# Performance work log

Hardware: AMD Instinct MI355X
Metric: run time of the kernel (lower is better)

The kernel has to match this reference:

```python
import jax, jax.numpy as jnp
import numpy as np

B, D, H = 16384, 1024, 4096


def setup_inputs() -> dict:
    key = jax.random.key(0)
    kx, kp, k1, k2 = jax.random.split(key, 4)
    X = jax.random.normal(kx, (B, D), dtype=jnp.float32)
    prot_col_idx = 3
    # protected column must be binary {0,1} so the remap produces no NaNs
    prot = jax.random.randint(kp, (B,), 0, 2).astype(jnp.float32)
    X = X.at[:, prot_col_idx].set(prot)
    W1 = jax.random.normal(k1, (D, H), dtype=jnp.float32) * (1.0 / np.sqrt(D))
    b1 = jnp.zeros((H,), dtype=jnp.float32)
    W2 = jax.random.normal(k2, (H, D), dtype=jnp.float32) * (1.0 / np.sqrt(H))
    b2 = jnp.zeros((D,), dtype=jnp.float32)
    return {"X": X, "W1": W1, "b1": b1, "W2": W2, "b2": b2,
            "prot_col_idx": prot_col_idx}


def reference(X, W1, b1, W2, b2, prot_col_idx):
    def explainer(x):
        h = jnp.tanh(x @ W1 + b1)          # [B, H]
        return h @ W2 + b2                  # [B, D]

    # vectorized remap of the protected column: 0 -> 1, 1 -> 0, else NaN
    col = X[:, prot_col_idx]
    flipped = jnp.where(col == 0, jnp.float32(1.0),
                        jnp.where(col == 1, jnp.float32(0.0), jnp.float32(jnp.nan)))
    X_copy = X.at[:, prot_col_idx].set(flipped.astype(X.dtype))

    shaps = explainer(X)
    shaps_counter = explainer(X_copy)
    mean_euclid_dist = jnp.mean(jnp.abs(shaps - shaps_counter), axis=0)  # [D]
    return mean_euclid_dist.sum()
```

## Files before the change

### kernel.cpp

```cpp
#include <hip/hip_runtime.h>
#include <stdint.h>

#define B_N 16384
#define D_N 1024
#define H_N 4096

typedef int i32x4 __attribute__((ext_vector_type(4)));
typedef int i32x8 __attribute__((ext_vector_type(8)));
typedef float f32x4 __attribute__((ext_vector_type(4)));

__device__ __forceinline__ void gload16(const void* g, void* l) {
  __builtin_amdgcn_global_load_lds((const __attribute__((address_space(1))) void*)g,
                                   (__attribute__((address_space(3))) void*)l,
                                   16, 0, 0);
}

__device__ __forceinline__ unsigned char f2fp8(float v) {
  return (unsigned char)(__builtin_amdgcn_cvt_pk_fp8_f32(v, v, 0, false) & 0xFF);
}

__device__ __forceinline__ int perm_h(int h) {
  return (h & ~63) | ((h & 15) << 2) | ((h >> 4) & 3);
}

__device__ __forceinline__ void transpose_tile(
    const float* __restrict__ in, unsigned char* __restrict__ out,
    int R, int C, float scale, float* __restrict__ w3, int pci,
    int i0, int j0, int tx, int ty, bool permute) {
  __shared__ float tile[32][33];
#pragma unroll
  for (int r = 0; r < 32; r += 8) {
    int i = i0 + ty + r;
    int j = j0 + tx;
    float v = in[(size_t)i * C + j];
    tile[ty + r][tx] = v;
    if (w3 != nullptr && i == pci) w3[j] = v;
  }
  __syncthreads();
#pragma unroll
  for (int r = 0; r < 32; r += 8) {
    int jo = j0 + ty + r;
    int io = i0 + tx;
    int ioo = permute ? perm_h(io) : io;
    out[(size_t)jo * R + ioo] = f2fp8(tile[tx][ty + r] * scale);
  }
}

__global__ __launch_bounds__(256) void prep_kernel(
    const float4* __restrict__ X4, int* __restrict__ Xb,
    float* __restrict__ s,
    const float* __restrict__ W1, unsigned char* __restrict__ W1T, float* __restrict__ w3,
    const float* __restrict__ W2, unsigned char* __restrict__ W2T,
    const int* __restrict__ pci_p, float* __restrict__ out0) {
  int b = blockIdx.x;
  int tid = threadIdx.x;
  int pci = *pci_p;
  if (b == 0 && tid == 0) out0[0] = 0.0f;
  if (b < 8192) {
    int i = (b * 256 + tid) * 2;
#pragma unroll
    for (int u = 0; u < 2; u++) {
      float4 v = X4[i + u];
      int p = __builtin_amdgcn_cvt_pk_fp8_f32(v.x, v.y, 0, false);
      p = __builtin_amdgcn_cvt_pk_fp8_f32(v.z, v.w, p, true);
      Xb[i + u] = p;
      if (((i + u) & (D_N / 4 - 1)) == (pci >> 2)) {
        int row = (i + u) >> 8;
        float c;
        switch (pci & 3) {
          case 0:  c = v.x; break;
          case 1:  c = v.y; break;
          case 2:  c = v.z; break;
          default: c = v.w; break;
        }
        s[row] = 1.0f - 2.0f * c;
      }
    }
  } else if (b < 12288) {
    int id = b - 8192;
    transpose_tile(W1, W1T, D_N, H_N, 16.0f, w3, pci,
                   (id >> 7) * 32, (id & 127) * 32, tid & 31, tid >> 5, false);
  } else {
    int id = b - 12288;
    transpose_tile(W2, W2T, H_N, D_N, 64.0f, nullptr, -1,
                   (id >> 5) * 32, (id & 31) * 32, tid & 31, tid >> 5, true);
  }
}

template <int KTOT>
__device__ __forceinline__ void mx_mainloop(
    const unsigned char* __restrict__ A, const unsigned char* __restrict__ B,
    int m0, int n0, int sa, int sb,
    unsigned char* As, unsigned char* Bs, f32x4 (&acc)[4][4]) {
  const int tid = threadIdx.x;
  const int lane = tid & 63;
  const int wave = tid >> 6;
  const int wm = (wave >> 1) * 64;
  const int wn = (wave & 1) * 64;
  const int lm = lane & 15;
  const int quad = lane >> 4;

  const int srow = tid >> 3;
  const int clog = (tid & 7) ^ (srow & 7);
  const unsigned char* Ag = A + (size_t)(m0 + srow) * KTOT + clog * 16;
  const unsigned char* Bg = B + (size_t)(n0 + srow) * KTOT + clog * 16;
  unsigned char* As_l = As + tid * 16;
  unsigned char* Bs_l = Bs + tid * 16;

  for (int k0 = 0; k0 < KTOT; k0 += 128) {
#pragma unroll
    for (int it = 0; it < 4; it++) {
      gload16(Ag + k0 + (size_t)(32 * it) * KTOT, As_l + it * 4096);
      gload16(Bg + k0 + (size_t)(32 * it) * KTOT, Bs_l + it * 4096);
    }
    __syncthreads();
    i32x8 b[4];
#pragma unroll
    for (int j = 0; j < 4; j++) {
      int r = wn + j * 16 + lm;
      int e = r & 7;
      i32x4 lo = *(const i32x4*)&Bs[r * 128 + ((2 * quad) ^ e) * 16];
      i32x4 hi = *(const i32x4*)&Bs[r * 128 + ((2 * quad + 1) ^ e) * 16];
      b[j] = __builtin_shufflevector(lo, hi, 0, 1, 2, 3, 4, 5, 6, 7);
    }
#pragma unroll
    for (int i = 0; i < 4; i++) {
      int r = wm + i * 16 + lm;
      int e = r & 7;
      i32x4 lo = *(const i32x4*)&As[r * 128 + ((2 * quad) ^ e) * 16];
      i32x4 hi = *(const i32x4*)&As[r * 128 + ((2 * quad + 1) ^ e) * 16];
      i32x8 av = __builtin_shufflevector(lo, hi, 0, 1, 2, 3, 4, 5, 6, 7);
#pragma unroll
      for (int j = 0; j < 4; j++)
        acc[i][j] = __builtin_amdgcn_mfma_scale_f32_16x16x128_f8f6f4(
            av, b[j], acc[i][j], 0, 0, 0, sa, 0, sb);
    }
    __syncthreads();
  }
}

__global__ __launch_bounds__(256, 4) void gemm1_dh(
    const unsigned char* __restrict__ Xb,
    const unsigned char* __restrict__ W1T,
    const float* __restrict__ b1,
    const float* __restrict__ w3,
    const float* __restrict__ s,
    unsigned int* __restrict__ Dh4) {
  __shared__ alignas(16) unsigned char As[128 * 128];
  __shared__ alignas(16) unsigned char Bs[128 * 128];
  int l = blockIdx.y * gridDim.x + blockIdx.x;
  int x = l & 7;
  int k = l >> 3;
  int ni = k & 7;
  int m  = (k >> 3) & 15;
  int nc = k >> 7;
  const int m0 = (x * 16 + m) * 128;
  const int n0 = (nc * 8 + ni) * 128;

  f32x4 acc[4][4] = {};
  mx_mainloop<D_N>(Xb, W1T, m0, n0, 127, 123, As, Bs, acc);

  const int tid = threadIdx.x;
  const int lane = tid & 63;
  const int wave = tid >> 6;
  const int wm = (wave >> 1) * 64;
  const int wn = (wave & 1) * 64;
  const int lm = lane & 15;
  const int quad = lane >> 4;

  float ewp[4], ewm[4], nump[4], numm[4], b1v[4];
#pragma unroll
  for (int j = 0; j < 4; j++) {
    int gh = n0 + wn + j * 16 + lm;
    float w = w3[gh];
    float ep = __expf(2.0f * w);
    float em = __expf(-2.0f * w);
    ewp[j] = ep; ewm[j] = em;
    nump[j] = 128.0f * (1.0f - ep);
    numm[j] = 128.0f * (1.0f - em);
    b1v[j] = b1[gh];
  }
  const size_t coloff = (size_t)((n0 + wn) >> 2) + lm;
#pragma unroll
  for (int i = 0; i < 4; i++) {
#pragma unroll
    for (int r = 0; r < 4; r++) {
      int gb = m0 + wm + i * 16 + quad * 4 + r;
      bool sp = s[gb] > 0.0f;
      float o[4];
#pragma unroll
      for (int j = 0; j < 4; j++) {
        float ews = sp ? ewp[j] : ewm[j];
        float num = sp ? nump[j] : numm[j];
        float z = fminf(acc[i][j][r] + b1v[j], 12.0f);
        float E = __expf(2.0f * z);
        float den = (E * ews + 1.0f) * (E + 1.0f);
        o[j] = (E * num) * __builtin_amdgcn_rcpf(den);
      }
      int p = __builtin_amdgcn_cvt_pk_fp8_f32(o[0], o[1], 0, false);
      p = __builtin_amdgcn_cvt_pk_fp8_f32(o[2], o[3], p, true);
      Dh4[(size_t)gb * (H_N / 4) + coloff] = (unsigned int)p;
    }
  }
}

__global__ __launch_bounds__(256, 4) void gemm2_abs(
    const unsigned char* __restrict__ Dh,
    const unsigned char* __restrict__ W2T,
    float* __restrict__ out) {
  __shared__ alignas(16) unsigned char As[128 * 128];
  __shared__ alignas(16) unsigned char Bs[128 * 128];
  __shared__ float wsum[4];
  int l = blockIdx.y * gridDim.x + blockIdx.x;
  int x = l & 7;
  int k = l >> 3;
  int c = k >> 6;
  int idx = k & 63;
  int m  = idx >> 2;
  int nj = idx & 3;
  const int m0 = (x * 16 + m) * 128;
  const int n0 = (c * 4 + nj) * 128;

  f32x4 acc[4][4] = {};
  mx_mainloop<H_N>(Dh, W2T, m0, n0, 121, 121, As, Bs, acc);

  const int tid = threadIdx.x;
  const int lane = tid & 63;
  const int wave = tid >> 6;

  float t = 0.0f;
#pragma unroll
  for (int i = 0; i < 4; i++)
#pragma unroll
    for (int j = 0; j < 4; j++)
#pragma unroll
      for (int r = 0; r < 4; r++)
        t += fabsf(acc[i][j][r]);

#pragma unroll
  for (int off2 = 32; off2 > 0; off2 >>= 1)
    t += __shfl_down(t, off2, 64);
  if (lane == 0) wsum[wave] = t;
  __syncthreads();
  if (tid == 0)
    atomicAdd(out, (wsum[0] + wsum[1] + wsum[2] + wsum[3]) * (1.0f / (float)B_N));
}

extern "C" void kernel_launch(void* const* d_in, const int* in_sizes, int n_in,
                              void* d_out, int out_size, void* d_ws, size_t ws_size,
                              hipStream_t stream) {
  const float* X  = (const float*)d_in[0];
  const float* W1 = (const float*)d_in[1];
  const float* b1 = (const float*)d_in[2];
  const float* W2 = (const float*)d_in[3];
  const int* pci  = (const int*)d_in[5];

  char* ws = (char*)d_ws;
  size_t off = 0;
  unsigned char* Xb  = (unsigned char*)(ws + off); off += (size_t)B_N * D_N;
  unsigned char* W1T = (unsigned char*)(ws + off); off += (size_t)H_N * D_N;
  unsigned char* W2T = (unsigned char*)(ws + off); off += (size_t)D_N * H_N;
  float* w3  = (float*)(ws + off); off += (size_t)H_N * 4;
  float* s   = (float*)(ws + off); off += (size_t)B_N * 4;
  unsigned char* Dh  = (unsigned char*)(ws + off); off += (size_t)B_N * H_N;
  if (ws_size < off) return;

  prep_kernel<<<16384, 256, 0, stream>>>((const float4*)X, (int*)Xb, s,
                                         W1, W1T, w3, W2, W2T, pci,
                                         (float*)d_out);
  gemm1_dh<<<dim3(32, 128), 256, 0, stream>>>(Xb, W1T, b1, w3, s,
                                              (unsigned int*)Dh);
  gemm2_abs<<<dim3(8, 128), 256, 0, stream>>>(Dh, W2T, (float*)d_out);
}
```

Before: 289.8 us.

## Use 256x256 tiles with 8 waves and double-buffered LDS prefetch in FP8 GEMMs

Both MX-FP8 GEMMs move from 128x128 tiles with 4 waves to 256x256 tiles with 8 waves, each wave computing 128x64. The main loop now double-buffers LDS and splits the next K-slab's global-to-LDS loads into chunks that are interleaved with the MFMA groups. It uses explicit vmcnt waits, barriers and s_setprio around the MFMA bursts. The aim is more operand reuse per byte loaded and hiding global load latency behind matrix math. The cost is 128KB of LDS per block, which allows only one block per CU, plus more barriers per K step; gemm2 launches just 256 blocks.

```diff
diff --git a/kernel.cpp b/kernel.cpp
--- a/kernel.cpp
+++ b/kernel.cpp
@@ -88,83 +88,135 @@
 }
 
 template <int KTOT>
-__device__ __forceinline__ void mx_mainloop(
+__device__ __forceinline__ void mx8_mainloop(
     const unsigned char* __restrict__ A, const unsigned char* __restrict__ B,
     int m0, int n0, int sa, int sb,
-    unsigned char* As, unsigned char* Bs, f32x4 (&acc)[4][4]) {
+    unsigned char* __restrict__ As, unsigned char* __restrict__ Bs,
+    f32x4 (&acc)[8][4]) {
+  static_assert(KTOT % 128 == 0, "KTOT must be a multiple of 128");
   const int tid = threadIdx.x;
   const int lane = tid & 63;
   const int wave = tid >> 6;
-  const int wm = (wave >> 1) * 64;
-  const int wn = (wave & 1) * 64;
+  const int wm = (wave >> 2) * 128;
+  const int wn = (wave & 3) * 64;
   const int lm = lane & 15;
   const int quad = lane >> 4;
 
   const int srow = tid >> 3;
-  const int clog = (tid & 7) ^ (srow & 7);
-  const unsigned char* Ag = A + (size_t)(m0 + srow) * KTOT + clog * 16;
-  const unsigned char* Bg = B + (size_t)(n0 + srow) * KTOT + clog * 16;
-  unsigned char* As_l = As + tid * 16;
-  unsigned char* Bs_l = Bs + tid * 16;
-
-  for (int k0 = 0; k0 < KTOT; k0 += 128) {
-#pragma unroll
-    for (int it = 0; it < 4; it++) {
-      gload16(Ag + k0 + (size_t)(32 * it) * KTOT, As_l + it * 4096);
-      gload16(Bg + k0 + (size_t)(32 * it) * KTOT, Bs_l + it * 4096);
-    }
-    __syncthreads();
-    i32x8 b[4];
-#pragma unroll
-    for (int j = 0; j < 4; j++) {
-      int r = wn + j * 16 + lm;
-      int e = r & 7;
-      i32x4 lo = *(const i32x4*)&Bs[r * 128 + ((2 * quad) ^ e) * 16];
-      i32x4 hi = *(const i32x4*)&Bs[r * 128 + ((2 * quad + 1) ^ e) * 16];
-      b[j] = __builtin_shufflevector(lo, hi, 0, 1, 2, 3, 4, 5, 6, 7);
-    }
-#pragma unroll
-    for (int i = 0; i < 4; i++) {
-      int r = wm + i * 16 + lm;
-      int e = r & 7;
-      i32x4 lo = *(const i32x4*)&As[r * 128 + ((2 * quad) ^ e) * 16];
-      i32x4 hi = *(const i32x4*)&As[r * 128 + ((2 * quad + 1) ^ e) * 16];
-      i32x8 av = __builtin_shufflevector(lo, hi, 0, 1, 2, 3, 4, 5, 6, 7);
-#pragma unroll
-      for (int j = 0; j < 4; j++)
-        acc[i][j] = __builtin_amdgcn_mfma_scale_f32_16x16x128_f8f6f4(
-            av, b[j], acc[i][j], 0, 0, 0, sa, 0, sb);
-    }
-    __syncthreads();
-  }
-}
-
-__global__ __launch_bounds__(256, 4) void gemm1_dh(
+  const int sg = tid & 7;
+  const unsigned char* Ag = A + (size_t)(m0 + srow) * KTOT + ((sg ^ (srow & 7)) * 16);
+  const unsigned char* Bg = B + (size_t)(n0 + srow) * KTOT + ((sg ^ (srow & 7)) * 16);
+  unsigned char* AsW = As + tid * 16;
+  unsigned char* BsW = Bs + tid * 16;
+
+#define STGA(c_, k_, p_) gload16(Ag + (k_) + (c_) * 64 * KTOT, AsW + (p_) * 32768 + (c_) * 8192)
+#define STGB(c_, k_, p_) gload16(Bg + (k_) + (c_) * 64 * KTOT, BsW + (p_) * 32768 + (c_) * 8192)
+#define LDF(d_, base_, r_) { \
+    const int rr_ = (r_); \
+    const int e_ = rr_ & 7; \
+    const unsigned char* pp_ = (base_) + rr_ * 128; \
+    i32x4 lo_ = *(const i32x4*)(pp_ + (((2 * quad) ^ e_) * 16)); \
+    i32x4 hi_ = *(const i32x4*)(pp_ + (((2 * quad + 1) ^ e_) * 16)); \
+    d_ = __builtin_shufflevector(lo_, hi_, 0, 1, 2, 3, 4, 5, 6, 7); }
+#define MF(a_, b_, c_) \
+    __builtin_amdgcn_mfma_scale_f32_16x16x128_f8f6f4((a_), (b_), (c_), 0, 0, 0, sa, 0, sb)
+#define FENCE() asm volatile("" ::: "memory")
+#define BARR() { FENCE(); __builtin_amdgcn_s_barrier(); FENCE(); }
+#define MM8(i0_, i1_, aA_, aB_) { \
+    __builtin_amdgcn_s_setprio(1); \
+    acc[i0_][0] = MF(aA_, b0, acc[i0_][0]); \
+    acc[i0_][1] = MF(aA_, b1, acc[i0_][1]); \
+    acc[i0_][2] = MF(aA_, b2, acc[i0_][2]); \
+    acc[i0_][3] = MF(aA_, b3, acc[i0_][3]); \
+    acc[i1_][0] = MF(aB_, b0, acc[i1_][0]); \
+    acc[i1_][1] = MF(aB_, b1, acc[i1_][1]); \
+    acc[i1_][2] = MF(aB_, b2, acc[i1_][2]); \
+    acc[i1_][3] = MF(aB_, b3, acc[i1_][3]); \
+    __builtin_amdgcn_s_setprio(0); }
+
+  STGB(0, 0, 0); STGB(1, 0, 0); STGB(2, 0, 0); STGB(3, 0, 0);
+  STGA(0, 0, 0); STGA(2, 0, 0);
+  STGA(1, 0, 0); STGA(3, 0, 0);
+  asm volatile("s_waitcnt vmcnt(2)" ::: "memory");
+  BARR();
+
+  const int NT = KTOT / 128;
+#pragma unroll 2
+  for (int t = 0; t < NT; ++t) {
+    const unsigned char* Ar = As + (t & 1) * 32768;
+    const unsigned char* Br = Bs + (t & 1) * 32768;
+    const int pq = (t & 1) ^ 1;
+    const int k1 = (t + 1) * 128;
+    const bool pf = (t + 1 < NT);
+
+    i32x8 b0, b1, b2, b3, av0, av1;
+    LDF(b0, Br, wn + lm);
+    LDF(b1, Br, wn + 16 + lm);
+    LDF(b2, Br, wn + 32 + lm);
+    LDF(b3, Br, wn + 48 + lm);
+    LDF(av0, Ar, wm + lm);
+    LDF(av1, Ar, wm + 16 + lm);
+    if (pf) { STGB(0, k1, pq); STGB(1, k1, pq); }
+    BARR();
+    MM8(0, 1, av0, av1);
+    BARR();
+
+    LDF(av0, Ar, wm + 32 + lm);
+    LDF(av1, Ar, wm + 48 + lm);
+    if (pf) { STGB(2, k1, pq); STGB(3, k1, pq); }
+    BARR();
+    MM8(2, 3, av0, av1);
+    if (pf) { asm volatile("s_waitcnt vmcnt(4)" ::: "memory"); }
+    else    { asm volatile("s_waitcnt vmcnt(0)" ::: "memory"); }
+    BARR();
+
+    LDF(av0, Ar, wm + 64 + lm);
+    LDF(av1, Ar, wm + 80 + lm);
+    if (pf) { STGA(0, k1, pq); STGA(2, k1, pq); }
+    BARR();
+    MM8(4, 5, av0, av1);
+    BARR();
+
+    LDF(av0, Ar, wm + 96 + lm);
+    LDF(av1, Ar, wm + 112 + lm);
+    if (pf) { STGA(1, k1, pq); STGA(3, k1, pq); }
+    BARR();
+    MM8(6, 7, av0, av1);
+    if (pf) { asm volatile("s_waitcnt vmcnt(2)" ::: "memory"); }
+    BARR();
+  }
+#undef STGA
+#undef STGB
+#undef LDF
+#undef MF
+#undef FENCE
+#undef BARR
+#undef MM8
+}
+
+__global__ __launch_bounds__(512, 2) void gemm1_dh(
     const unsigned char* __restrict__ Xb,
     const unsigned char* __restrict__ W1T,
     const float* __restrict__ b1,
     const float* __restrict__ w3,
     const float* __restrict__ s,
     unsigned int* __restrict__ Dh4) {
-  __shared__ alignas(16) unsigned char As[128 * 128];
-  __shared__ alignas(16) unsigned char Bs[128 * 128];
-  int l = blockIdx.y * gridDim.x + blockIdx.x;
-  int x = l & 7;
-  int k = l >> 3;
-  int ni = k & 7;
-  int m  = (k >> 3) & 15;
-  int nc = k >> 7;
-  const int m0 = (x * 16 + m) * 128;
-  const int n0 = (nc * 8 + ni) * 128;
-
-  f32x4 acc[4][4] = {};
-  mx_mainloop<D_N>(Xb, W1T, m0, n0, 127, 123, As, Bs, acc);
+  __shared__ alignas(16) unsigned char As[65536];
+  __shared__ alignas(16) unsigned char Bs[65536];
+  const int l = blockIdx.x;
+  const int x = l & 7;
+  const int k = l >> 3;
+  const int m0 = (x * 8 + (k & 7)) * 256;
+  const int n0 = (k >> 3) * 256;
+
+  f32x4 acc[8][4] = {};
+  mx8_mainloop<D_N>(Xb, W1T, m0, n0, 127, 123, As, Bs, acc);
 
   const int tid = threadIdx.x;
   const int lane = tid & 63;
   const int wave = tid >> 6;
-  const int wm = (wave >> 1) * 64;
-  const int wn = (wave & 1) * 64;
+  const int wm = (wave >> 2) * 128;
+  const int wn = (wave & 3) * 64;
   const int lm = lane & 15;
   const int quad = lane >> 4;
 
@@ -182,7 +234,7 @@
   }
   const size_t coloff = (size_t)((n0 + wn) >> 2) + lm;
 #pragma unroll
-  for (int i = 0; i < 4; i++) {
+  for (int i = 0; i < 8; i++) {
 #pragma unroll
     for (int r = 0; r < 4; r++) {
       int gb = m0 + wm + i * 16 + quad * 4 + r;
@@ -204,25 +256,21 @@
   }
 }
 
-__global__ __launch_bounds__(256, 4) void gemm2_abs(
+__global__ __launch_bounds__(512, 2) void gemm2_abs(
     const unsigned char* __restrict__ Dh,
     const unsigned char* __restrict__ W2T,
     float* __restrict__ out) {
-  __shared__ alignas(16) unsigned char As[128 * 128];
-  __shared__ alignas(16) unsigned char Bs[128 * 128];
-  __shared__ float wsum[4];
-  int l = blockIdx.y * gridDim.x + blockIdx.x;
-  int x = l & 7;
-  int k = l >> 3;
-  int c = k >> 6;
-  int idx = k & 63;
-  int m  = idx >> 2;
-  int nj = idx & 3;
-  const int m0 = (x * 16 + m) * 128;
-  const int n0 = (c * 4 + nj) * 128;
-
-  f32x4 acc[4][4] = {};
-  mx_mainloop<H_N>(Dh, W2T, m0, n0, 121, 121, As, Bs, acc);
+  __shared__ alignas(16) unsigned char As[65536];
+  __shared__ alignas(16) unsigned char Bs[65536];
+  __shared__ float wsum[8];
+  const int l = blockIdx.x;
+  const int x = l & 7;
+  const int k = l >> 3;
+  const int m0 = (x * 8 + (k & 7)) * 256;
+  const int n0 = (k >> 3) * 256;
+
+  f32x4 acc[8][4] = {};
+  mx8_mainloop<H_N>(Dh, W2T, m0, n0, 121, 121, As, Bs, acc);
 
   const int tid = threadIdx.x;
   const int lane = tid & 63;
@@ -230,7 +278,7 @@
 
   float t = 0.0f;
 #pragma unroll
-  for (int i = 0; i < 4; i++)
+  for (int i = 0; i < 8; i++)
 #pragma unroll
     for (int j = 0; j < 4; j++)
 #pragma unroll
@@ -242,8 +290,12 @@
     t += __shfl_down(t, off2, 64);
   if (lane == 0) wsum[wave] = t;
   __syncthreads();
-  if (tid == 0)
-    atomicAdd(out, (wsum[0] + wsum[1] + wsum[2] + wsum[3]) * (1.0f / (float)B_N));
+  if (tid == 0) {
+    float tt = 0.0f;
+#pragma unroll
+    for (int w = 0; w < 8; w++) tt += wsum[w];
+    atomicAdd(out, tt * (1.0f / (float)B_N));
+  }
 }
 
 extern "C" void kernel_launch(void* const* d_in, const int* in_sizes, int n_in,
@@ -268,7 +320,6 @@
   prep_kernel<<<16384, 256, 0, stream>>>((const float4*)X, (int*)Xb, s,
                                          W1, W1T, w3, W2, W2T, pci,
                                          (float*)d_out);
-  gemm1_dh<<<dim3(32, 128), 256, 0, stream>>>(Xb, W1T, b1, w3, s,
-                                              (unsigned int*)Dh);
-  gemm2_abs<<<dim3(8, 128), 256, 0, stream>>>(Dh, W2T, (float*)d_out);
-}
+  gemm1_dh<<<1024, 512, 0, stream>>>(Xb, W1T, b1, w3, s, (unsigned int*)Dh);
+  gemm2_abs<<<256, 512, 0, stream>>>(Dh, W2T, (float*)d_out);
+}
```

After: 717.9 us. 2.48x slower.

## Double-buffer A tile in LDS and load B fragments directly from global

Applied to the files above, without the earlier changes.

The shared GEMM mainloop now keeps two LDS buffers for the A tile and prefetches the next K-slice asynchronously while the current one is computed, using explicit vmcnt waits and barriers. B operand fragments are read straight from global memory into registers instead of being staged through LDS. The aim is to overlap global loads with MFMA work and cut LDS traffic. In exchange, B global reads are uncoalesced per-lane loads that may stall if their latency isn't hidden, and the hand-tuned waitcnt accounting is fragile.

```diff
diff --git a/kernel.cpp b/kernel.cpp
--- a/kernel.cpp
+++ b/kernel.cpp
@@ -88,10 +88,10 @@
 }
 
 template <int KTOT>
-__device__ __forceinline__ void mx_mainloop(
-    const unsigned char* __restrict__ A, const unsigned char* __restrict__ B,
+__device__ __forceinline__ void mx_bd_mainloop(
+    const unsigned char* __restrict__ A, const unsigned char* __restrict__ Bm,
     int m0, int n0, int sa, int sb,
-    unsigned char* As, unsigned char* Bs, f32x4 (&acc)[4][4]) {
+    unsigned char* __restrict__ As, f32x4 (&acc)[4][4]) {
   const int tid = threadIdx.x;
   const int lane = tid & 63;
   const int wave = tid >> 6;
@@ -101,42 +101,66 @@
   const int quad = lane >> 4;
 
   const int srow = tid >> 3;
-  const int clog = (tid & 7) ^ (srow & 7);
-  const unsigned char* Ag = A + (size_t)(m0 + srow) * KTOT + clog * 16;
-  const unsigned char* Bg = B + (size_t)(n0 + srow) * KTOT + clog * 16;
-  unsigned char* As_l = As + tid * 16;
-  unsigned char* Bs_l = Bs + tid * 16;
-
-  for (int k0 = 0; k0 < KTOT; k0 += 128) {
-#pragma unroll
-    for (int it = 0; it < 4; it++) {
-      gload16(Ag + k0 + (size_t)(32 * it) * KTOT, As_l + it * 4096);
-      gload16(Bg + k0 + (size_t)(32 * it) * KTOT, Bs_l + it * 4096);
-    }
-    __syncthreads();
-    i32x8 b[4];
-#pragma unroll
-    for (int j = 0; j < 4; j++) {
-      int r = wn + j * 16 + lm;
-      int e = r & 7;
-      i32x4 lo = *(const i32x4*)&Bs[r * 128 + ((2 * quad) ^ e) * 16];
-      i32x4 hi = *(const i32x4*)&Bs[r * 128 + ((2 * quad + 1) ^ e) * 16];
-      b[j] = __builtin_shufflevector(lo, hi, 0, 1, 2, 3, 4, 5, 6, 7);
-    }
-#pragma unroll
-    for (int i = 0; i < 4; i++) {
-      int r = wm + i * 16 + lm;
-      int e = r & 7;
-      i32x4 lo = *(const i32x4*)&As[r * 128 + ((2 * quad) ^ e) * 16];
-      i32x4 hi = *(const i32x4*)&As[r * 128 + ((2 * quad + 1) ^ e) * 16];
-      i32x8 av = __builtin_shufflevector(lo, hi, 0, 1, 2, 3, 4, 5, 6, 7);
-#pragma unroll
-      for (int j = 0; j < 4; j++)
-        acc[i][j] = __builtin_amdgcn_mfma_scale_f32_16x16x128_f8f6f4(
-            av, b[j], acc[i][j], 0, 0, 0, sa, 0, sb);
-    }
-    __syncthreads();
-  }
+  const int sg = tid & 7;
+  const unsigned char* Ag = A + (size_t)(m0 + srow) * KTOT + ((sg ^ (srow & 7)) * 16);
+  unsigned char* AsW = As + tid * 16;
+
+  const int e = lm & 7;
+  const unsigned char* Ard_lo = As + (wm + lm) * 128 + (((2 * quad) ^ e) * 16);
+  const unsigned char* Ard_hi = As + (wm + lm) * 128 + (((2 * quad + 1) ^ e) * 16);
+
+  const unsigned char* Bg0 = Bm + (size_t)(n0 + wn + lm) * KTOT + 32 * quad;
+
+  i32x8 b0, b1, b2, b3;
+
+#define STG(it_, kn_, p_) gload16(Ag + (kn_) + (size_t)(32 * (it_)) * KTOT, \
+                                  AsW + (p_) * 16384 + (it_) * 4096)
+#define LDBG(d_, j_, kn_) { \
+    const unsigned char* p_ = Bg0 + (size_t)(j_) * 16 * KTOT + (kn_); \
+    i32x4 lo_ = *(const i32x4*)(p_); \
+    i32x4 hi_ = *(const i32x4*)(p_ + 16); \
+    d_ = __builtin_shufflevector(lo_, hi_, 0, 1, 2, 3, 4, 5, 6, 7); }
+#define LDA(d_, i_, P_) { \
+    i32x4 lo_ = *(const i32x4*)(Ard_lo + (P_) * 16384 + (i_) * 2048); \
+    i32x4 hi_ = *(const i32x4*)(Ard_hi + (P_) * 16384 + (i_) * 2048); \
+    d_ = __builtin_shufflevector(lo_, hi_, 0, 1, 2, 3, 4, 5, 6, 7); }
+#define MF(a_, b_, c_) \
+    __builtin_amdgcn_mfma_scale_f32_16x16x128_f8f6f4((a_), (b_), (c_), 0, 0, 0, sa, 0, sb)
+#define BARR() { asm volatile("" ::: "memory"); __builtin_amdgcn_s_barrier(); \
+                 asm volatile("" ::: "memory"); }
+#define ROW(i_, P_) { i32x8 a_; LDA(a_, i_, P_); \
+    acc[i_][0] = MF(a_, b0, acc[i_][0]); \
+    acc[i_][1] = MF(a_, b1, acc[i_][1]); \
+    acc[i_][2] = MF(a_, b2, acc[i_][2]); \
+    acc[i_][3] = MF(a_, b3, acc[i_][3]); }
+
+  STG(0, 0, 0); STG(1, 0, 0); STG(2, 0, 0); STG(3, 0, 0);
+  LDBG(b0, 0, 0); LDBG(b1, 1, 0); LDBG(b2, 2, 0); LDBG(b3, 3, 0);
+
+  const int NT = KTOT / 128;
+#pragma unroll 1
+  for (int t = 0; t < NT; ++t) {
+    const int P = t & 1;
+    const bool pf = (t + 1 < NT);
+    const int kn = (t + 1) * 128;
+    if (pf) { STG(0, kn, 1 - P); STG(1, kn, 1 - P);
+              STG(2, kn, 1 - P); STG(3, kn, 1 - P); }
+    if (pf) { asm volatile("s_waitcnt vmcnt(4)" ::: "memory"); }
+    else    { asm volatile("s_waitcnt vmcnt(0)" ::: "memory"); }
+    BARR();
+    ROW(0, P); ROW(1, P); ROW(2, P); ROW(3, P);
+    __builtin_amdgcn_sched_barrier(0);
+    if (pf) { LDBG(b0, 0, kn); LDBG(b1, 1, kn);
+              LDBG(b2, 2, kn); LDBG(b3, 3, kn); }
+    BARR();
+  }
+
+#undef STG
+#undef LDBG
+#undef LDA
+#undef MF
+#undef BARR
+#undef ROW
 }
 
 __global__ __launch_bounds__(256, 4) void gemm1_dh(
@@ -146,8 +170,7 @@
     const float* __restrict__ w3,
     const float* __restrict__ s,
     unsigned int* __restrict__ Dh4) {
-  __shared__ alignas(16) unsigned char As[128 * 128];
-  __shared__ alignas(16) unsigned char Bs[128 * 128];
+  __shared__ alignas(16) unsigned char As[32768];
   int l = blockIdx.y * gridDim.x + blockIdx.x;
   int x = l & 7;
   int k = l >> 3;
@@ -158,7 +181,7 @@
   const int n0 = (nc * 8 + ni) * 128;
 
   f32x4 acc[4][4] = {};
-  mx_mainloop<D_N>(Xb, W1T, m0, n0, 127, 123, As, Bs, acc);
+  mx_bd_mainloop<D_N>(Xb, W1T, m0, n0, 127, 123, As, acc);
 
   const int tid = threadIdx.x;
   const int lane = tid & 63;
@@ -208,8 +231,7 @@
     const unsigned char* __restrict__ Dh,
     const unsigned char* __restrict__ W2T,
     float* __restrict__ out) {
-  __shared__ alignas(16) unsigned char As[128 * 128];
-  __shared__ alignas(16) unsigned char Bs[128 * 128];
+  __shared__ alignas(16) unsigned char As[32768];
   __shared__ float wsum[4];
   int l = blockIdx.y * gridDim.x + blockIdx.x;
   int x = l & 7;
@@ -222,7 +244,7 @@
   const int n0 = (c * 4 + nj) * 128;
 
   f32x4 acc[4][4] = {};
-  mx_mainloop<H_N>(Dh, W2T, m0, n0, 121, 121, As, Bs, acc);
+  mx_bd_mainloop<H_N>(Dh, W2T, m0, n0, 121, 121, As, acc);
 
   const int tid = threadIdx.x;
   const int lane = tid & 63;
```

New measurement: 943.5 us. +225.5%, slower.
